# Kernel optimization log

Measured on AMD Instinct MI355X. Metric: run time of the kernel, lower is better.

The kernel has to match this reference:

```python
import jax, jax.numpy as jnp
import numpy as np
import math

NUM_HEADS = 8
EMB = 256

def setup_inputs() -> dict:
    key = jax.random.key(0)
    ks = jax.random.split(key, 9)
    B_, N, C = 1024, 64, EMB  # 16 images * 64 windows, 8x8 window, C=256
    nW = 64
    q = jax.random.normal(ks[0], (B_, N, C), dtype=jnp.float32)
    k = jax.random.normal(ks[1], (B_, N, C), dtype=jnp.float32)
    v = jax.random.normal(ks[2], (B_, N, C), dtype=jnp.float32)
    mask = jax.random.normal(ks[3], (nW, N, N), dtype=jnp.float32)
    # MLP params (Linear: y = x @ W^T + b; we store W already transposed for x @ W)
    hid = 4 * C
    s1 = 1.0 / math.sqrt(C)
    s2 = 1.0 / math.sqrt(hid)
    w1 = jax.random.uniform(ks[4], (C, hid), minval=-s1, maxval=s1, dtype=jnp.float32)
    b1 = jax.random.uniform(ks[5], (hid,), minval=-s1, maxval=s1, dtype=jnp.float32)
    w2 = jax.random.uniform(ks[6], (hid, C), minval=-s2, maxval=s2, dtype=jnp.float32)
    b2 = jax.random.uniform(ks[7], (C,), minval=-s2, maxval=s2, dtype=jnp.float32)
    return {"q": q, "k": k, "v": v, "mask": mask, "H": 64, "W": 64,
            "w1": w1, "b1": b1, "w2": w2, "b2": b2}

def reference(q, k, v, mask, H, W, w1, b1, w2, b2):
    B_, N, C = q.shape
    h = NUM_HEADS
    d = C // h
    # separate heads: (B_, h, N, d)
    qh = q.reshape(B_, N, h, d).transpose(0, 2, 1, 3)
    kh = k.reshape(B_, N, h, d).transpose(0, 2, 1, 3)
    vh = v.reshape(B_, N, h, d).transpose(0, 2, 1, 3)
    attn = jnp.einsum('bhnd,bhmd->bhnm', qh, kh)  # raw scores
    nW = mask.shape[0]
    # additive window mask BEFORE scaling (faithful to original order)
    attn = attn.reshape(B_ // nW, nW, h, N, N) + mask[None, :, None, :, :]
    attn = attn.reshape(B_, h, N, N) / math.sqrt(d)
    attn = jax.nn.softmax(attn, axis=-1)
    out = jnp.einsum('bhnm,bhmd->bhnd', attn, vh)
    out = out.transpose(0, 2, 1, 3).reshape(B_, N, C)  # recombine heads
    # linear Mlp (dropout is identity at p=0.0); torch nn.GELU is exact erf
    hmid = jax.nn.gelu(out @ w1 + b1, approximate=False)
    out = out + (hmid @ w2 + b2)
    return out
```

## Files before the change

### kernel.cpp

```cpp
#include <hip/hip_runtime.h>
#include <hip/hip_bf16.h>
#include <cstdint>
#include <cstddef>

typedef __attribute__((ext_vector_type(8))) short bf16x8;
typedef __attribute__((ext_vector_type(4))) float f32x4;

static __device__ __forceinline__ unsigned short f2bf(float f) {
    __hip_bfloat16 h = __float2bfloat16(f);
    return *reinterpret_cast<unsigned short*>(&h);
}

static __device__ __forceinline__ f32x4 mfma_bf16(bf16x8 a, bf16x8 b, f32x4 c) {
    return __builtin_amdgcn_mfma_f32_16x16x32_bf16(a, b, c, 0, 0, 0);
}

static __device__ __forceinline__ bf16x8 pack8(float4 a, float4 b) {
    bf16x8 f;
    f[0]=(short)f2bf(a.x); f[1]=(short)f2bf(a.y); f[2]=(short)f2bf(a.z); f[3]=(short)f2bf(a.w);
    f[4]=(short)f2bf(b.x); f[5]=(short)f2bf(b.y); f[6]=(short)f2bf(b.z); f[7]=(short)f2bf(b.w);
    return f;
}

static __device__ __forceinline__ float gelu_erf(float v) {
    float s = v * 0.70710678118654752f;
    float a = fabsf(s);
    float t = __builtin_amdgcn_rcpf(1.0f + 0.3275911f * a);
    float poly = ((((1.061405429f * t - 1.453152027f) * t + 1.421413741f) * t
                   - 0.284496736f) * t + 0.254829592f) * t;
    float e = 1.0f - poly * __expf(-a * a);
    float erfv = copysignf(e, s);
    return 0.5f * v * (1.0f + erfv);
}

static __device__ __forceinline__ void load_lds16(const unsigned short* g, unsigned short* l) {
    __builtin_amdgcn_global_load_lds(
        (const __attribute__((address_space(1))) unsigned int*)g,
        (__attribute__((address_space(3))) unsigned int*)l, 16, 0, 0);
}

__global__ __launch_bounds__(256) void attn_kernel(
    const float* __restrict__ q, const float* __restrict__ k,
    const float* __restrict__ v, const float* __restrict__ mask,
    float* __restrict__ xout)
{
    __shared__ unsigned short Qs[64][40];
    __shared__ unsigned short Ks[64][40];
    __shared__ unsigned short Vt[32][72];
    __shared__ unsigned short Ps[64][72];

    const int tid  = threadIdx.x;
    const int b    = blockIdx.x >> 3;
    const int h    = blockIdx.x & 7;
    const int lane = tid & 63;
    const int l15  = lane & 15;
    const int g    = lane >> 4;
    const int w    = tid >> 6;

    {
        int row = tid >> 2;
        int seg = tid & 3;
        size_t base = ((size_t)(b * 64 + row)) * 256 + h * 32 + seg * 8;

        float4 a0 = *(const float4*)(q + base);
        float4 a1 = *(const float4*)(q + base + 4);
        unsigned short* p = &Qs[row][seg * 8];
        p[0]=f2bf(a0.x); p[1]=f2bf(a0.y); p[2]=f2bf(a0.z); p[3]=f2bf(a0.w);
        p[4]=f2bf(a1.x); p[5]=f2bf(a1.y); p[6]=f2bf(a1.z); p[7]=f2bf(a1.w);

        a0 = *(const float4*)(k + base);
        a1 = *(const float4*)(k + base + 4);
        p = &Ks[row][seg * 8];
        p[0]=f2bf(a0.x); p[1]=f2bf(a0.y); p[2]=f2bf(a0.z); p[3]=f2bf(a0.w);
        p[4]=f2bf(a1.x); p[5]=f2bf(a1.y); p[6]=f2bf(a1.z); p[7]=f2bf(a1.w);

        a0 = *(const float4*)(v + base);
        a1 = *(const float4*)(v + base + 4);
        int c = seg * 8;
        Vt[c + 0][row] = f2bf(a0.x);
        Vt[c + 1][row] = f2bf(a0.y);
        Vt[c + 2][row] = f2bf(a0.z);
        Vt[c + 3][row] = f2bf(a0.w);
        Vt[c + 4][row] = f2bf(a1.x);
        Vt[c + 5][row] = f2bf(a1.y);
        Vt[c + 6][row] = f2bf(a1.z);
        Vt[c + 7][row] = f2bf(a1.w);
    }
    __syncthreads();

    f32x4 s[4];
    {
        bf16x8 aQ = *(const bf16x8*)&Qs[w * 16 + l15][g * 8];
        #pragma unroll
        for (int ct = 0; ct < 4; ++ct) {
            bf16x8 bK = *(const bf16x8*)&Ks[ct * 16 + l15][g * 8];
            f32x4 z = {0.f, 0.f, 0.f, 0.f};
            s[ct] = mfma_bf16(aQ, bK, z);
        }
    }

    const float* mbase = mask + (size_t)(b & 63) * 4096;
    const float INV = 0.17677669529663688f;
    float rsum[4];
    #pragma unroll
    for (int r = 0; r < 4; ++r) {
        int row = w * 16 + g * 4 + r;
        float pr[4];
        #pragma unroll
        for (int ct = 0; ct < 4; ++ct)
            pr[ct] = (s[ct][r] + mbase[row * 64 + ct * 16 + l15]) * INV;
        float m = fmaxf(fmaxf(pr[0], pr[1]), fmaxf(pr[2], pr[3]));
        #pragma unroll
        for (int off = 1; off < 16; off <<= 1)
            m = fmaxf(m, __shfl_xor(m, off));
        float sum = 0.f;
        #pragma unroll
        for (int ct = 0; ct < 4; ++ct) { pr[ct] = __expf(pr[ct] - m); sum += pr[ct]; }
        #pragma unroll
        for (int off = 1; off < 16; off <<= 1)
            sum += __shfl_xor(sum, off);
        rsum[r] = sum;
        #pragma unroll
        for (int ct = 0; ct < 4; ++ct)
            Ps[row][ct * 16 + l15] = f2bf(pr[ct]);
    }

    f32x4 o[2] = {};
    #pragma unroll
    for (int ks = 0; ks < 2; ++ks) {
        bf16x8 pa = *(const bf16x8*)&Ps[w * 16 + l15][ks * 32 + g * 8];
        #pragma unroll
        for (int n = 0; n < 2; ++n) {
            bf16x8 vb = *(const bf16x8*)&Vt[n * 16 + l15][ks * 32 + g * 8];
            o[n] = mfma_bf16(pa, vb, o[n]);
        }
    }

    #pragma unroll
    for (int n = 0; n < 2; ++n) {
        #pragma unroll
        for (int r = 0; r < 4; ++r) {
            int row = w * 16 + g * 4 + r;
            xout[((size_t)(b * 64 + row)) * 256 + h * 32 + n * 16 + l15] =
                o[n][r] / rsum[r];
        }
    }
}

__global__ __launch_bounds__(256) void prep_w1(const float* __restrict__ src,
                                               unsigned short* __restrict__ dst)
{
    __shared__ float tile[64][65];
    const int kt = blockIdx.x, nb = blockIdx.y;
    const int t = threadIdx.x;
    const int r0 = t >> 4, c4 = (t & 15) * 4;
    #pragma unroll
    for (int p = 0; p < 4; ++p) {
        int kk = r0 + p * 16;
        float4 d = *(const float4*)(src + (size_t)(kt * 64 + kk) * 1024 + nb * 64 + c4);
        tile[kk][c4+0]=d.x; tile[kk][c4+1]=d.y; tile[kk][c4+2]=d.z; tile[kk][c4+3]=d.w;
    }
    __syncthreads();
    #pragma unroll
    for (int i = 0; i < 2; ++i) {
        int f = t + 256 * i;
        int ksl = f >> 8;
        int ntg = (f >> 6) & 3;
        int gv  = (f >> 4) & 3;
        int l15v = f & 15;
        int n_local = ntg * 16 + l15v;
        int k_local = ksl * 32 + gv * 8;
        int c  = nb * 2 + (ntg >> 1);
        int nt = ntg & 1;
        int ks = kt * 2 + ksl;
        unsigned short tmp[8];
        #pragma unroll
        for (int e = 0; e < 8; ++e) tmp[e] = f2bf(tile[k_local + e][n_local]);
        size_t off = (size_t)c * 8192 + (size_t)((ks * 2 + nt) * 512)
                   + (gv * 16 + l15v) * 8;
        *(bf16x8*)(dst + off) = *(const bf16x8*)tmp;
    }
}

__global__ __launch_bounds__(256) void prep_w2(const float* __restrict__ src,
                                               unsigned short* __restrict__ dst)
{
    __shared__ float tile[64][65];
    const int ob = blockIdx.x, kb = blockIdx.y;
    const int t = threadIdx.x;
    const int r0 = t >> 4, c4 = (t & 15) * 4;
    #pragma unroll
    for (int p = 0; p < 4; ++p) {
        int kk = r0 + p * 16;
        float4 d = *(const float4*)(src + (size_t)(kb * 64 + kk) * 256 + ob * 64 + c4);
        tile[kk][c4+0]=d.x; tile[kk][c4+1]=d.y; tile[kk][c4+2]=d.z; tile[kk][c4+3]=d.w;
    }
    __syncthreads();
    #pragma unroll
    for (int i = 0; i < 2; ++i) {
        int f = t + 256 * i;
        int ksl = f >> 8;
        int tq  = (f >> 6) & 3;
        int gv  = (f >> 4) & 3;
        int l15v = f & 15;
        int c_local = tq * 16 + l15v;
        int k_local = ksl * 32 + gv * 8;
        int c = kb * 2 + ksl;
        unsigned short tmp[8];
        #pragma unroll
        for (int e = 0; e < 8; ++e) tmp[e] = f2bf(tile[k_local + e][c_local]);
        size_t off = (size_t)c * 8192 + (size_t)((ob * 4 + tq) * 512)
                   + (gv * 16 + l15v) * 8;
        *(bf16x8*)(dst + off) = *(const bf16x8*)tmp;
    }
}

__global__ __launch_bounds__(512, 4) void mlp_fused(
    const float* __restrict__ xin, float* __restrict__ xio,
    const unsigned short* __restrict__ wt1, const float* __restrict__ b1,
    const unsigned short* __restrict__ wt2, const float* __restrict__ b2)
{
    __shared__ unsigned short w1c[2][8192];
    __shared__ unsigned short w2c[2][8192];
    __shared__ unsigned short Hs[8][16][36];
    __shared__ float b1s[1024];

    const int tid  = threadIdx.x;
    const int lane = tid & 63;
    const int l15  = lane & 15;
    const int g    = lane >> 4;
    const int wid  = tid >> 6;
    const int fb   = (g * 16 + l15) * 8;

    const size_t rowbase = (size_t)blockIdx.x * 128;

    auto stage = [&](const unsigned short* gbase, unsigned short* lbase) {
        #pragma unroll
        for (int i = 0; i < 2; ++i) {
            load_lds16(gbase + (i * 512 + tid) * 8,
                       lbase + (i * 512 + wid * 64) * 8);
        }
    };

    stage(wt1, &w1c[0][0]);
    stage(wt2, &w2c[0][0]);

    b1s[tid]       = b1[tid];
    b1s[tid + 512] = b1[tid + 512];

    bf16x8 xf[8];
    {
        const float* xr = xin + (rowbase + wid * 16 + l15) * 256;
        #pragma unroll
        for (int ks = 0; ks < 8; ++ks) {
            float4 a0 = *(const float4*)(xr + ks * 32 + g * 8);
            float4 a1 = *(const float4*)(xr + ks * 32 + g * 8 + 4);
            xf[ks] = pack8(a0, a1);
        }
    }

    f32x4 oacc[16] = {};

    for (int hc = 0; hc < 32; ++hc) {
        const int cur = hc & 1;
        __syncthreads();

        if (hc < 31) {
            stage(wt1 + (size_t)(hc + 1) * 8192, &w1c[cur ^ 1][0]);
            stage(wt2 + (size_t)(hc + 1) * 8192, &w2c[cur ^ 1][0]);
        }

        f32x4 hacc[2] = {};
        #pragma unroll
        for (int ks = 0; ks < 8; ++ks) {
            bf16x8 b0  = *(const bf16x8*)&w1c[cur][(ks * 2 + 0) * 512 + fb];
            bf16x8 b1f = *(const bf16x8*)&w1c[cur][(ks * 2 + 1) * 512 + fb];
            hacc[0] = mfma_bf16(xf[ks], b0,  hacc[0]);
            hacc[1] = mfma_bf16(xf[ks], b1f, hacc[1]);
        }

        #pragma unroll
        for (int nt = 0; nt < 2; ++nt) {
            int coll = nt * 16 + l15;
            float bias = b1s[hc * 32 + coll];
            #pragma unroll
            for (int r = 0; r < 4; ++r) {
                float vv = gelu_erf(hacc[nt][r] + bias);
                Hs[wid][g * 4 + r][coll] = f2bf(vv);
            }
        }

        bf16x8 aH = *(const bf16x8*)&Hs[wid][l15][g * 8];
        #pragma unroll
        for (int n = 0; n < 16; ++n) {
            bf16x8 bF = *(const bf16x8*)&w2c[cur][n * 512 + fb];
            oacc[n] = mfma_bf16(aH, bF, oacc[n]);
        }
    }

    #pragma unroll
    for (int n = 0; n < 16; ++n) {
        int col = n * 16 + l15;
        float bias = b2[col];
        #pragma unroll
        for (int r = 0; r < 4; ++r) {
            size_t idx = (rowbase + wid * 16 + g * 4 + r) * 256 + col;
            xio[idx] = oacc[n][r] + bias + xio[idx];
        }
    }
}

extern "C" void kernel_launch(void* const* d_in, const int* in_sizes, int n_in,
                              void* d_out, int out_size, void* d_ws, size_t ws_size,
                              hipStream_t stream)
{
    const float* q    = (const float*)d_in[0];
    const float* k    = (const float*)d_in[1];
    const float* v    = (const float*)d_in[2];
    const float* mask = (const float*)d_in[3];
    const float* w1   = (const float*)d_in[6];
    const float* b1   = (const float*)d_in[7];
    const float* w2   = (const float*)d_in[8];
    const float* b2   = (const float*)d_in[9];

    float* xio = (float*)d_out;

    unsigned short* wt1 = (unsigned short*)d_ws;
    unsigned short* wt2 = wt1 + (size_t)1024 * 256;

    prep_w1<<<dim3(4, 16), 256, 0, stream>>>(w1, wt1);
    prep_w2<<<dim3(4, 16), 256, 0, stream>>>(w2, wt2);

    attn_kernel<<<8192, 256, 0, stream>>>(q, k, v, mask, xio);

    mlp_fused<<<512, 512, 0, stream>>>(xio, xio, wt1, b1, wt2, b2);
}
```

Baseline: 170.0 us.

## Keep GELU hidden tile in registers by transposing first MFMA and permuting W1

Swaps the operands of the first GEMM's MFMA so each lane's accumulator already holds the hidden values in the A-operand layout needed by the second MFMA. The W1 prep kernel permutes hidden columns so each lane gets eight contiguous hidden units. This removes the per-warp LDS staging buffer Hs, its stores and its reload. The cost is a more intricate column permutation that must match the bias indexing exactly.

```diff
diff --git a/kernel.cpp b/kernel.cpp
--- a/kernel.cpp
+++ b/kernel.cpp
@@ -164,14 +164,14 @@
     #pragma unroll
     for (int i = 0; i < 2; ++i) {
         int f = t + 256 * i;
-        int ksl = f >> 8;
-        int ntg = (f >> 6) & 3;
-        int gv  = (f >> 4) & 3;
-        int l15v = f & 15;
-        int n_local = ntg * 16 + l15v;
+        int chalf = f >> 8;
+        int ksl   = (f >> 7) & 1;
+        int nt    = (f >> 6) & 1;
+        int gv    = (f >> 4) & 3;
+        int l15v  = f & 15;
+        int n_local = chalf * 32 + 8 * (l15v >> 2) + 4 * nt + (l15v & 3);
         int k_local = ksl * 32 + gv * 8;
-        int c  = nb * 2 + (ntg >> 1);
-        int nt = ntg & 1;
+        int c  = nb * 2 + chalf;
         int ks = kt * 2 + ksl;
         unsigned short tmp[8];
         #pragma unroll
@@ -222,7 +222,6 @@
 {
     __shared__ unsigned short w1c[2][8192];
     __shared__ unsigned short w2c[2][8192];
-    __shared__ unsigned short Hs[8][16][36];
     __shared__ float b1s[1024];
 
     const int tid  = threadIdx.x;
@@ -273,24 +272,25 @@
         f32x4 hacc[2] = {};
         #pragma unroll
         for (int ks = 0; ks < 8; ++ks) {
-            bf16x8 b0  = *(const bf16x8*)&w1c[cur][(ks * 2 + 0) * 512 + fb];
-            bf16x8 b1f = *(const bf16x8*)&w1c[cur][(ks * 2 + 1) * 512 + fb];
-            hacc[0] = mfma_bf16(xf[ks], b0,  hacc[0]);
-            hacc[1] = mfma_bf16(xf[ks], b1f, hacc[1]);
-        }
-
-        #pragma unroll
-        for (int nt = 0; nt < 2; ++nt) {
-            int coll = nt * 16 + l15;
-            float bias = b1s[hc * 32 + coll];
-            #pragma unroll
-            for (int r = 0; r < 4; ++r) {
-                float vv = gelu_erf(hacc[nt][r] + bias);
-                Hs[wid][g * 4 + r][coll] = f2bf(vv);
-            }
-        }
-
-        bf16x8 aH = *(const bf16x8*)&Hs[wid][l15][g * 8];
+            bf16x8 w0 = *(const bf16x8*)&w1c[cur][(ks * 2 + 0) * 512 + fb];
+            bf16x8 w1f = *(const bf16x8*)&w1c[cur][(ks * 2 + 1) * 512 + fb];
+            hacc[0] = mfma_bf16(w0,  xf[ks], hacc[0]);
+            hacc[1] = mfma_bf16(w1f, xf[ks], hacc[1]);
+        }
+
+        const float* bp = &b1s[hc * 32 + g * 8];
+        float4 ba = *(const float4*)bp;
+        float4 bb = *(const float4*)(bp + 4);
+        bf16x8 aH;
+        aH[0] = (short)f2bf(gelu_erf(hacc[0][0] + ba.x));
+        aH[1] = (short)f2bf(gelu_erf(hacc[0][1] + ba.y));
+        aH[2] = (short)f2bf(gelu_erf(hacc[0][2] + ba.z));
+        aH[3] = (short)f2bf(gelu_erf(hacc[0][3] + ba.w));
+        aH[4] = (short)f2bf(gelu_erf(hacc[1][0] + bb.x));
+        aH[5] = (short)f2bf(gelu_erf(hacc[1][1] + bb.y));
+        aH[6] = (short)f2bf(gelu_erf(hacc[1][2] + bb.z));
+        aH[7] = (short)f2bf(gelu_erf(hacc[1][3] + bb.w));
+
         #pragma unroll
         for (int n = 0; n < 16; ++n) {
             bf16x8 bF = *(const bf16x8*)&w2c[cur][n * 512 + fb];
```

New measurement: 170.0 us. About the same (+0.0%).
